# Kernel optimization log

Hardware: AMD Instinct MI355X
Metric: run time of the kernel (lower is better)

Reference implementation:

```python
import jax, jax.numpy as jnp
import numpy as np

NUM_HEADS = 8


def setup_inputs() -> dict:
    key = jax.random.key(0)
    k1, k2, k3 = jax.random.split(key, 3)
    B, N, C = 4, 8448, 512
    x = jax.random.normal(k1, (B, N, C), dtype=jnp.float32)
    w_qkv = jax.random.normal(k2, (3 * C, C), dtype=jnp.float32) * (C ** -0.5)
    w_proj = jax.random.normal(k3, (C, C), dtype=jnp.float32) * (C ** -0.5)
    b_proj = jnp.zeros((C,), dtype=jnp.float32)
    return {"x": x, "w_qkv": w_qkv, "w_proj": w_proj, "b_proj": b_proj, "N_points": 8192}


def reference(x, w_qkv, w_proj, b_proj, N_points):
    B, N, C = x.shape
    H = NUM_HEADS
    hd = C // H
    scale = hd ** -0.5
    N_latent = N - N_points

    qkv = (x @ w_qkv.T).reshape(B, N, 3, H, hd).transpose(2, 0, 3, 1, 4)  # [3,B,H,N,hd]
    q, k, v = qkv[0], qkv[1], qkv[2]
    q_l, k_l, v_l = q[:, :, :N_latent], k[:, :, :N_latent], v[:, :, :N_latent]
    q_p, k_p, v_p = q[:, :, N_latent:], k[:, :, N_latent:], v[:, :, N_latent:]

    # joint cross+self attention for the points
    attn_cross = jnp.einsum('bhpd,bhld->bhpl', q_p, k_l) * scale        # [B,H,P,L]
    attn_self = jnp.sum(q_p * k_p, axis=-1, keepdims=True) * scale      # [B,H,P,1]
    attn_joint = jax.nn.softmax(jnp.concatenate([attn_cross, attn_self], axis=-1), axis=-1)

    sum_cross = jnp.einsum('bhpl,bhld->bhpd', attn_joint[..., :N_latent], v_l)
    sum_self = attn_joint[..., N_latent:] * v_p
    out_points = (sum_cross + sum_self).transpose(0, 2, 1, 3).reshape(B, N_points, C)

    # standard self-attention over latent tokens
    attn_latent = jax.nn.softmax(jnp.einsum('bhqd,bhkd->bhqk', q_l, k_l) * scale, axis=-1)
    out_latent = jnp.einsum('bhqk,bhkd->bhqd', attn_latent, v_l).transpose(0, 2, 1, 3).reshape(B, N_latent, C)

    output = jnp.concatenate([out_latent, out_points], axis=1) @ w_proj.T + b_proj
    attn_mean = attn_joint[..., :-1].mean(axis=1)  # [B,P,L]
    return output, attn_mean
```

## Files before the change

kernel.cpp:

```cpp
#include <hip/hip_runtime.h>

#define BQ 4
#define NH 8
#define NTOK 8448
#define NLAT 256
#define NPTS 8192
#define CDIM 512
#define HD 64
#define SCALE 0.125f

typedef __attribute__((ext_vector_type(8))) short short8b;
typedef __attribute__((ext_vector_type(4))) float f32x4;

static __device__ __forceinline__ float4 ld4(const float* p) { return *(const float4*)p; }

static __device__ __forceinline__ short f2b(float f) {
  union { float f; unsigned u; } c; c.f = f;
  unsigned u = c.u;
  u += ((u >> 16) & 1u) + 0x7fffu;
  return (short)(u >> 16);
}

static __device__ __forceinline__ float b2f(unsigned short u) {
  union { unsigned u; float f; } c; c.u = ((unsigned)u) << 16; return c.f;
}

static __device__ __forceinline__ int cvtpk(float lo, float hi) {
  int r; asm("v_cvt_pk_bf16_f32 %0, %1, %2" : "=v"(r) : "v"(lo), "v"(hi)); return r;
}

static __device__ __forceinline__ void gload_lds16(const unsigned short* g, unsigned short* l) {
  __builtin_amdgcn_global_load_lds((const __attribute__((address_space(1))) void*)g,
                                   (__attribute__((address_space(3))) void*)l, 16, 0, 0);
}

__global__ __launch_bounds__(256) void to_bf16_3(const float* __restrict__ a, unsigned short* __restrict__ ao_, int na8,
                                                 const float* __restrict__ b, unsigned short* __restrict__ bo, int nb8,
                                                 const float* __restrict__ c, unsigned short* __restrict__ co, int nc8) {
  int i = blockIdx.x * 256 + threadIdx.x;
  const float* src; unsigned short* dst; int idx;
  if (i < na8) { src = a; dst = ao_; idx = i; }
  else if (i < na8 + nb8) { src = b; dst = bo; idx = i - na8; }
  else if (i < na8 + nb8 + nc8) { src = c; dst = co; idx = i - na8 - nb8; }
  else return;
  float4 x0 = ld4(src + (size_t)idx * 8);
  float4 x1 = ld4(src + (size_t)idx * 8 + 4);
  short8b r;
  r[0] = f2b(x0.x); r[1] = f2b(x0.y); r[2] = f2b(x0.z); r[3] = f2b(x0.w);
  r[4] = f2b(x1.x); r[5] = f2b(x1.y); r[6] = f2b(x1.z); r[7] = f2b(x1.w);
  *(short8b*)&dst[(size_t)idx * 8] = r;
}

#define STAGE128(PA, PB, kt, s)                                                              \
  do {                                                                                       \
    const int _c = (kt) * 64 + scell;                                                        \
    unsigned short* _d = &lds[(s) * 16384 + t * 8];                                          \
    gload_lds16((PA) + (size_t)(m0 + sr) * CDIM + _c,       _d);                             \
    gload_lds16((PA) + (size_t)(m0 + 32 + sr) * CDIM + _c,  _d + 2048);                      \
    gload_lds16((PA) + (size_t)(m0 + 64 + sr) * CDIM + _c,  _d + 4096);                      \
    gload_lds16((PA) + (size_t)(m0 + 96 + sr) * CDIM + _c,  _d + 6144);                      \
    gload_lds16((PB) + (size_t)(j0 + sr) * CDIM + _c,       _d + 8192);                      \
    gload_lds16((PB) + (size_t)(j0 + 32 + sr) * CDIM + _c,  _d + 10240);                     \
    gload_lds16((PB) + (size_t)(j0 + 64 + sr) * CDIM + _c,  _d + 12288);                     \
    gload_lds16((PB) + (size_t)(j0 + 96 + sr) * CDIM + _c,  _d + 14336);                     \
  } while (0)

#define GEMM128_BODY(PA, PB)                                                                 \
  __shared__ unsigned short lds[32768];                                                      \
  const int fl = blockIdx.y * gridDim.x + blockIdx.x;                                        \
  const int nchunk = (gridDim.x * gridDim.y) >> 3;                                           \
  const int wid = (fl & 7) * nchunk + (fl >> 3);                                             \
  const int m0 = (wid / gridDim.x) * 128;                                                    \
  const int j0 = (wid % gridDim.x) * 128;                                                    \
  const int t = threadIdx.x;                                                                 \
  const int lane = t & 63, wave = t >> 6;                                                    \
  const int wr = wave >> 1, wc = wave & 1;                                                   \
  const int lm = lane & 15, lq = lane >> 4;                                                  \
  const int sr = t >> 3;                                                                     \
  const int scell = (((t & 7) ^ (sr & 7)) << 3);                                             \
  f32x4 acc[4][4] = {};                                                                      \
  STAGE128(PA, PB, 0, 0);                                                                    \
  STAGE128(PA, PB, 1, 1);                                                                    \
  for (int kt = 0; kt < 8; ++kt) {                                                           \
    const int s = kt & 1;                                                                    \
    if (kt == 7) asm volatile("s_waitcnt vmcnt(0)" ::: "memory");                            \
    else         asm volatile("s_waitcnt vmcnt(8)" ::: "memory");                            \
    __builtin_amdgcn_s_barrier();                                                            \
    const unsigned short* sb = &lds[s * 16384];                                              \
    short8b af[4][2], bf[4][2];                                                              \
    _Pragma("unroll")                                                                        \
    for (int mt = 0; mt < 4; ++mt) {                                                         \
      const int RA = wr * 64 + mt * 16 + lm;                                                 \
      const int RB = wc * 64 + mt * 16 + lm;                                                 \
      af[mt][0] = *(const short8b*)&sb[RA * 64 + ((lq ^ (RA & 7)) << 3)];                    \
      af[mt][1] = *(const short8b*)&sb[RA * 64 + (((4 | lq) ^ (RA & 7)) << 3)];              \
      bf[mt][0] = *(const short8b*)&sb[8192 + RB * 64 + ((lq ^ (RB & 7)) << 3)];             \
      bf[mt][1] = *(const short8b*)&sb[8192 + RB * 64 + (((4 | lq) ^ (RB & 7)) << 3)];       \
    }                                                                                        \
    __builtin_amdgcn_s_setprio(1);                                                           \
    _Pragma("unroll")                                                                        \
    for (int ks = 0; ks < 2; ++ks)                                                           \
      _Pragma("unroll")                                                                      \
      for (int mt = 0; mt < 4; ++mt)                                                         \
        _Pragma("unroll")                                                                    \
        for (int nt = 0; nt < 4; ++nt)                                                       \
          acc[mt][nt] = __builtin_amdgcn_mfma_f32_16x16x32_bf16(af[mt][ks], bf[nt][ks],      \
                                                                acc[mt][nt], 0, 0, 0);       \
    __builtin_amdgcn_s_setprio(0);                                                           \
    asm volatile("s_waitcnt lgkmcnt(0)" ::: "memory");                                       \
    __builtin_amdgcn_s_barrier();                                                            \
    __builtin_amdgcn_sched_barrier(0);                                                       \
    if (kt < 6) STAGE128(PA, PB, kt + 2, s);                                                 \
  }

__global__ __launch_bounds__(256, 2) void qkv_mfma(const unsigned short* __restrict__ xb,
                                                   const unsigned short* __restrict__ wb,
                                                   unsigned short* __restrict__ qo,
                                                   unsigned short* __restrict__ ko,
                                                   unsigned short* __restrict__ vo) {
  GEMM128_BODY(xb, wb)
  const int s_ = j0 >> 9;
  unsigned short* dst = (s_ == 0) ? qo : ((s_ == 1) ? ko : vo);
  const int b = m0 / NTOK;
  const int n0 = m0 % NTOK;
  const int h = ((j0 >> 6) + wc) & 7;
#pragma unroll
  for (int mt = 0; mt < 4; ++mt) {
#pragma unroll
    for (int r = 0; r < 4; ++r) {
      const int n = n0 + wr * 64 + mt * 16 + lq * 4 + r;
      const size_t ob = (((size_t)b * NH + h) * NTOK + n) * HD;
#pragma unroll
      for (int nt = 0; nt < 4; ++nt)
        dst[ob + nt * 16 + lm] = (unsigned short)f2b(acc[mt][nt][r]);
    }
  }
}

__global__ __launch_bounds__(256, 2) void proj_mfma(const unsigned short* __restrict__ ab,
                                                    const unsigned short* __restrict__ wpb,
                                                    const float* __restrict__ bias,
                                                    float* __restrict__ out) {
  GEMM128_BODY(ab, wpb)
#pragma unroll
  for (int mt = 0; mt < 4; ++mt) {
#pragma unroll
    for (int r = 0; r < 4; ++r) {
      const int m = m0 + wr * 64 + mt * 16 + lq * 4 + r;
#pragma unroll
      for (int nt = 0; nt < 4; ++nt) {
        const int j = j0 + wc * 64 + nt * 16 + lm;
        out[(size_t)m * CDIM + j] = acc[mt][nt][r] + bias[j];
      }
    }
  }
}

__global__ __launch_bounds__(512, 2) void attn_pm(const unsigned short* __restrict__ qb,
                                                  const unsigned short* __restrict__ kb,
                                                  const unsigned short* __restrict__ vb,
                                                  unsigned short* __restrict__ aob,
                                                  float* __restrict__ out1) {
  __shared__ unsigned short kl[2][16384];
  __shared__ unsigned short vt[2][16384];
  const int t = threadIdx.x;
  const int lane = t & 63, wave = t >> 6;
  const int lm = lane & 15, lq = lane >> 4;
  if (blockIdx.x < 64) {
    const int idx = blockIdx.x;
    const int bh = idx >> 1, half = idx & 1;
    const size_t bhb = (size_t)bh * NTOK * HD;
    {
      const int vr = t >> 1, dh = t & 1;
      const unsigned short* vg = vb + bhb + (size_t)vr * HD + dh * 32;
      short8b rv[4];
#pragma unroll
      for (int i = 0; i < 4; ++i) rv[i] = *(const short8b*)(vg + i * 8);
      const int gsw = vr >> 3, wi = vr & 7;
#pragma unroll
      for (int i = 0; i < 4; ++i) {
        const int d0 = dh * 4 + i;
#pragma unroll
        for (int j = 0; j < 8; ++j)
          vt[0][(d0 * 8 + j) * 256 + ((gsw ^ j) << 3) + wi] = (unsigned short)rv[i][j];
      }
    }
    __syncthreads();
    const int b = bh >> 3, h = bh & 7;
    const int q0 = half * 128 + wave * 16;
    const size_t qrow = bhb + (size_t)(q0 + lm) * HD;
    const short8b bq0 = *(const short8b*)(qb + qrow + lq * 8);
    const short8b bq1 = *(const short8b*)(qb + qrow + 32 + lq * 8);
    f32x4 s[16] = {};
    __builtin_amdgcn_s_setprio(1);
#pragma unroll
    for (int mt = 0; mt < 16; ++mt) {
      const int krow = ((mt >> 1) << 5) + ((lm >> 2) << 3) + ((mt & 1) << 2) + (lm & 3);
      const unsigned short* kr = kb + bhb + (size_t)krow * HD + lq * 8;
      s[mt] = __builtin_amdgcn_mfma_f32_16x16x32_bf16(*(const short8b*)kr, bq0, s[mt], 0, 0, 0);
      s[mt] = __builtin_amdgcn_mfma_f32_16x16x32_bf16(*(const short8b*)(kr + 32), bq1, s[mt], 0, 0, 0);
    }
    __builtin_amdgcn_s_setprio(0);
    float mx = -1e30f;
#pragma unroll
    for (int mt = 0; mt < 16; ++mt)
#pragma unroll
      for (int r = 0; r < 4; ++r) mx = fmaxf(mx, s[mt][r]);
    mx = fmaxf(mx, __shfl_xor(mx, 16));
    mx = fmaxf(mx, __shfl_xor(mx, 32));
    const float m = mx * SCALE;
    float sum = 0.f;
#pragma unroll
    for (int mt = 0; mt < 16; ++mt)
#pragma unroll
      for (int r = 0; r < 4; ++r) {
        float e = __expf(fmaf(s[mt][r], SCALE, -m));
        s[mt][r] = e;
        sum += e;
      }
    sum += __shfl_xor(sum, 16);
    sum += __shfl_xor(sum, 32);
    const float inv = 1.f / sum;
#pragma unroll
    for (int mt = 0; mt < 16; ++mt)
#pragma unroll
      for (int r = 0; r < 4; ++r) s[mt][r] *= inv;
    f32x4 o[4] = {};
    __builtin_amdgcn_s_setprio(1);
#pragma unroll
    for (int ks = 0; ks < 8; ++ks) {
      union { int i[4]; short8b v; } af;
      af.i[0] = cvtpk(s[2 * ks][0], s[2 * ks][1]);
      af.i[1] = cvtpk(s[2 * ks][2], s[2 * ks][3]);
      af.i[2] = cvtpk(s[2 * ks + 1][0], s[2 * ks + 1][1]);
      af.i[3] = cvtpk(s[2 * ks + 1][2], s[2 * ks + 1][3]);
#pragma unroll
      for (int ntd = 0; ntd < 4; ++ntd) {
        const int row = ntd * 16 + lm;
        const short8b bv = *(const short8b*)&vt[0][row * 256 + ((((ks << 2) | lq) ^ (lm & 7)) << 3)];
        o[ntd] = __builtin_amdgcn_mfma_f32_16x16x32_bf16(af.v, bv, o[ntd], 0, 0, 0);
      }
    }
    __builtin_amdgcn_s_setprio(0);
#pragma unroll
    for (int ntd = 0; ntd < 4; ++ntd)
#pragma unroll
      for (int r = 0; r < 4; ++r) {
        const int n = q0 + lq * 4 + r;
        aob[((size_t)b * NTOK + n) * CDIM + h * HD + ntd * 16 + lm] =
            (unsigned short)f2b(o[ntd][r]);
      }
    return;
  }
  const int bidx = blockIdx.x - 64;
  const int b = bidx >> 6, pq = bidx & 63;
  const int pp0 = pq * 128 + wave * 16;
  const size_t bb = (size_t)(b * NH) * NTOK * HD;
  const int vr = t >> 1, dh = t & 1;
  const int gsw = vr >> 3, wi = vr & 7;
  short8b vregs[4];
#define ISSUE_K(hh, sl_)                                                          \
  do {                                                                            \
    const unsigned short* kg = kb + bb + (size_t)(hh) * NTOK * HD;                \
    _Pragma("unroll")                                                             \
    for (int c = 0; c < 4; ++c) {                                                 \
      const int rr = c * 64 + (t >> 3);                                           \
      const int mt_ = rr >> 4, w_ = rr & 15;                                      \
      const int g = 32 * (mt_ >> 1) + 8 * (w_ >> 2) + 4 * (mt_ & 1) + (w_ & 3);   \
      gload_lds16(kg + g * HD + (((t & 7) ^ (rr & 7)) << 3),                      \
                  &kl[sl_][(c * 512 + t) * 8]);                                   \
    }                                                                             \
  } while (0)
#define READ_V(hh)                                                                \
  do {                                                                            \
    const unsigned short* vg = vb + bb + (size_t)(hh) * NTOK * HD +               \
                               (size_t)vr * HD + dh * 32;                         \
    _Pragma("unroll")                                                             \
    for (int i = 0; i < 4; ++i) vregs[i] = *(const short8b*)(vg + i * 8);         \
  } while (0)
#define WRITE_V(sl_)                                                              \
  do {                                                                            \
    _Pragma("unroll")                                                             \
    for (int i = 0; i < 4; ++i) {                                                 \
      const int d0 = dh * 4 + i;                                                  \
      _Pragma("unroll")                                                           \
      for (int j = 0; j < 8; ++j)                                                 \
        vt[sl_][(d0 * 8 + j) * 256 + ((gsw ^ j) << 3) + wi] =                     \
            (unsigned short)vregs[i][j];                                          \
    }                                                                             \
  } while (0)
  f32x4 prob[16] = {};
  ISSUE_K(0, 0); READ_V(0);
  asm volatile("s_waitcnt vmcnt(0)" ::: "memory");
  WRITE_V(0);
  ISSUE_K(1, 1); READ_V(1);
  __syncthreads();
  for (int h = 0; h < NH; ++h) {
    const int sl = h & 1;
    const size_t hb = bb + (size_t)h * NTOK * HD;
    const size_t qrow = hb + (size_t)(NLAT + pp0 + lm) * HD;
    const short8b bq0 = *(const short8b*)(qb + qrow + lq * 8);
    const short8b bq1 = *(const short8b*)(qb + qrow + 32 + lq * 8);
    f32x4 s[16] = {};
    __builtin_amdgcn_s_setprio(1);
#pragma unroll
    for (int mt = 0; mt < 16; ++mt) {
      const int rr = mt * 16 + lm;
      const short8b ak0 = *(const short8b*)&kl[sl][rr * 64 + ((lq ^ (rr & 7)) << 3)];
      const short8b ak1 = *(const short8b*)&kl[sl][rr * 64 + (((4 | lq) ^ (rr & 7)) << 3)];
      s[mt] = __builtin_amdgcn_mfma_f32_16x16x32_bf16(ak0, bq0, s[mt], 0, 0, 0);
      s[mt] = __builtin_amdgcn_mfma_f32_16x16x32_bf16(ak1, bq1, s[mt], 0, 0, 0);
    }
    __builtin_amdgcn_s_setprio(0);
    float sself = 0.f;
    {
      const unsigned short* qp = qb + qrow + lq * 16;
      const unsigned short* kp = kb + qrow + lq * 16;
      short8b q0 = *(const short8b*)qp, q1 = *(const short8b*)(qp + 8);
      short8b k0 = *(const short8b*)kp, k1 = *(const short8b*)(kp + 8);
#pragma unroll
      for (int j = 0; j < 8; ++j)
        sself += b2f((unsigned short)q0[j]) * b2f((unsigned short)k0[j]) +
                 b2f((unsigned short)q1[j]) * b2f((unsigned short)k1[j]);
    }
    sself += __shfl_xor(sself, 16);
    sself += __shfl_xor(sself, 32);
    sself *= SCALE;
    float mx = -1e30f;
#pragma unroll
    for (int mt = 0; mt < 16; ++mt)
#pragma unroll
      for (int r = 0; r < 4; ++r) mx = fmaxf(mx, s[mt][r]);
    mx = fmaxf(mx, __shfl_xor(mx, 16));
    mx = fmaxf(mx, __shfl_xor(mx, 32));
    const float m = fmaxf(mx * SCALE, sself);
    float sum = 0.f;
#pragma unroll
    for (int mt = 0; mt < 16; ++mt)
#pragma unroll
      for (int r = 0; r < 4; ++r) {
        float e = __expf(fmaf(s[mt][r], SCALE, -m));
        s[mt][r] = e;
        sum += e;
      }
    sum += __shfl_xor(sum, 16);
    sum += __shfl_xor(sum, 32);
    const float pself = __expf(sself - m);
    const float inv = 1.f / (sum + pself);
#pragma unroll
    for (int mt = 0; mt < 16; ++mt)
#pragma unroll
      for (int r = 0; r < 4; ++r) {
        const float pn = s[mt][r] * inv;
        s[mt][r] = pn;
        prob[mt][r] += pn;
      }
    f32x4 o[4] = {};
    __builtin_amdgcn_s_setprio(1);
#pragma unroll
    for (int ks = 0; ks < 8; ++ks) {
      union { int i[4]; short8b v; } af;
      af.i[0] = cvtpk(s[2 * ks][0], s[2 * ks][1]);
      af.i[1] = cvtpk(s[2 * ks][2], s[2 * ks][3]);
      af.i[2] = cvtpk(s[2 * ks + 1][0], s[2 * ks + 1][1]);
      af.i[3] = cvtpk(s[2 * ks + 1][2], s[2 * ks + 1][3]);
#pragma unroll
      for (int ntd = 0; ntd < 4; ++ntd) {
        const int row = ntd * 16 + lm;
        const short8b bv = *(const short8b*)&vt[sl][row * 256 + ((((ks << 2) | lq) ^ (lm & 7)) << 3)];
        o[ntd] = __builtin_amdgcn_mfma_f32_16x16x32_bf16(af.v, bv, o[ntd], 0, 0, 0);
      }
    }
    __builtin_amdgcn_s_setprio(0);
    const float pisl = pself * inv;
    float psl[4];
#pragma unroll
    for (int r = 0; r < 4; ++r) psl[r] = __shfl(pisl, lq * 4 + r);
#pragma unroll
    for (int ntd = 0; ntd < 4; ++ntd)
#pragma unroll
      for (int r = 0; r < 4; ++r) {
        const int n = NLAT + pp0 + lq * 4 + r;
        const float v_ = b2f(vb[hb + (size_t)n * HD + ntd * 16 + lm]);
        aob[((size_t)b * NTOK + n) * CDIM + h * HD + ntd * 16 + lm] =
            (unsigned short)f2b(o[ntd][r] + psl[r] * v_);
      }
    __syncthreads();
    if (h < 7) {
      asm volatile("s_waitcnt vmcnt(0)" ::: "memory");
      WRITE_V(sl ^ 1);
      if (h < 6) { ISSUE_K(h + 2, sl); READ_V(h + 2); }
      __syncthreads();
    }
  }
  const size_t orow = ((size_t)b * NPTS + pp0 + lm) * NLAT;
#pragma unroll
  for (int mt = 0; mt < 16; ++mt) {
    const int col = 32 * (mt >> 1) + 8 * lq + 4 * (mt & 1);
    *(float4*)&out1[orow + col] = make_float4(prob[mt][0] * 0.125f, prob[mt][1] * 0.125f,
                                              prob[mt][2] * 0.125f, prob[mt][3] * 0.125f);
  }
#undef ISSUE_K
#undef READ_V
#undef WRITE_V
}

extern "C" void kernel_launch(void* const* d_in, const int* in_sizes, int n_in,
                              void* d_out, int out_size, void* d_ws, size_t ws_size,
                              hipStream_t stream) {
  const float* x      = (const float*)d_in[0];
  const float* w_qkv  = (const float*)d_in[1];
  const float* w_proj = (const float*)d_in[2];
  const float* b_proj = (const float*)d_in[3];
  const size_t QSZ = (size_t)BQ * NH * NTOK * HD;
  unsigned short* qb  = (unsigned short*)d_ws;
  unsigned short* kb  = qb + QSZ;
  unsigned short* vb  = kb + QSZ;
  unsigned short* aob = vb + QSZ;
  unsigned short* xb  = aob + QSZ;
  unsigned short* wb  = xb + QSZ;
  unsigned short* wpb = wb + 786432;
  float* out0 = (float*)d_out;
  float* out1 = out0 + (size_t)BQ * NTOK * CDIM;

  to_bf16_3<<<8960, 256, 0, stream>>>(x, xb, 2162688, w_qkv, wb, 98304, w_proj, wpb, 32768);
  qkv_mfma<<<dim3(12, 264), 256, 0, stream>>>(xb, wb, qb, kb, vb);
  attn_pm<<<320, 512, 0, stream>>>(qb, kb, vb, aob, out1);
  proj_mfma<<<dim3(4, 264), 256, 0, stream>>>(aob, wpb, b_proj, out0);
}
```

Baseline: 184.6 us.

## Single-buffer K/V LDS to double occupancy, reorder blocks, use exp2 softmax

Drops the double-buffered K and V shared-memory tiles in the fused attention kernel to a single buffer and raises launch bounds from 2 to 4 blocks per CU, so more waves can hide latency. The next head's K is now loaded only after a barrier at the end of each head, which removes the prefetch overlap across heads. Point blocks are remapped so neighbouring block IDs spread across batch and query chunks, and the latent blocks move to the end of the grid. Softmax switches from __expf to exp2f with log2(e) folded into the scale.

```diff
diff --git a/kernel.cpp b/kernel.cpp
--- a/kernel.cpp
+++ b/kernel.cpp
@@ -8,6 +8,8 @@
 #define CDIM 512
 #define HD 64
 #define SCALE 0.125f
+#define L2E 1.4426950408889634f
+#define SC2 0.1803368801111204f
 
 typedef __attribute__((ext_vector_type(8))) short short8b;
 typedef __attribute__((ext_vector_type(4))) float f32x4;
@@ -156,18 +158,18 @@
   }
 }
 
-__global__ __launch_bounds__(512, 2) void attn_pm(const unsigned short* __restrict__ qb,
+__global__ __launch_bounds__(512, 4) void attn_pm(const unsigned short* __restrict__ qb,
                                                   const unsigned short* __restrict__ kb,
                                                   const unsigned short* __restrict__ vb,
                                                   unsigned short* __restrict__ aob,
                                                   float* __restrict__ out1) {
-  __shared__ unsigned short kl[2][16384];
-  __shared__ unsigned short vt[2][16384];
+  __shared__ unsigned short kl[16384];
+  __shared__ unsigned short vt[16384];
   const int t = threadIdx.x;
   const int lane = t & 63, wave = t >> 6;
   const int lm = lane & 15, lq = lane >> 4;
-  if (blockIdx.x < 64) {
-    const int idx = blockIdx.x;
+  if (blockIdx.x >= 256) {
+    const int idx = blockIdx.x - 256;
     const int bh = idx >> 1, half = idx & 1;
     const size_t bhb = (size_t)bh * NTOK * HD;
     {
@@ -182,7 +184,7 @@
         const int d0 = dh * 4 + i;
 #pragma unroll
         for (int j = 0; j < 8; ++j)
-          vt[0][(d0 * 8 + j) * 256 + ((gsw ^ j) << 3) + wi] = (unsigned short)rv[i][j];
+          vt[(d0 * 8 + j) * 256 + ((gsw ^ j) << 3) + wi] = (unsigned short)rv[i][j];
       }
     }
     __syncthreads();
@@ -208,13 +210,13 @@
       for (int r = 0; r < 4; ++r) mx = fmaxf(mx, s[mt][r]);
     mx = fmaxf(mx, __shfl_xor(mx, 16));
     mx = fmaxf(mx, __shfl_xor(mx, 32));
-    const float m = mx * SCALE;
+    const float m2 = mx * SCALE * L2E;
     float sum = 0.f;
 #pragma unroll
     for (int mt = 0; mt < 16; ++mt)
 #pragma unroll
       for (int r = 0; r < 4; ++r) {
-        float e = __expf(fmaf(s[mt][r], SCALE, -m));
+        float e = exp2f(fmaf(s[mt][r], SC2, -m2));
         s[mt][r] = e;
         sum += e;
       }
@@ -237,7 +239,7 @@
 #pragma unroll
       for (int ntd = 0; ntd < 4; ++ntd) {
         const int row = ntd * 16 + lm;
-        const short8b bv = *(const short8b*)&vt[0][row * 256 + ((((ks << 2) | lq) ^ (lm & 7)) << 3)];
+        const short8b bv = *(const short8b*)&vt[row * 256 + ((((ks << 2) | lq) ^ (lm & 7)) << 3)];
         o[ntd] = __builtin_amdgcn_mfma_f32_16x16x32_bf16(af.v, bv, o[ntd], 0, 0, 0);
       }
     }
@@ -252,14 +254,15 @@
       }
     return;
   }
-  const int bidx = blockIdx.x - 64;
-  const int b = bidx >> 6, pq = bidx & 63;
+  const int fl = blockIdx.x;
+  const int wid = (fl & 7) * 32 + (fl >> 3);
+  const int b = wid >> 6, pq = wid & 63;
   const int pp0 = pq * 128 + wave * 16;
   const size_t bb = (size_t)(b * NH) * NTOK * HD;
   const int vr = t >> 1, dh = t & 1;
   const int gsw = vr >> 3, wi = vr & 7;
   short8b vregs[4];
-#define ISSUE_K(hh, sl_)                                                          \
+#define ISSUE_K(hh)                                                               \
   do {                                                                            \
     const unsigned short* kg = kb + bb + (size_t)(hh) * NTOK * HD;                \
     _Pragma("unroll")                                                             \
@@ -267,8 +270,7 @@
       const int rr = c * 64 + (t >> 3);                                           \
       const int mt_ = rr >> 4, w_ = rr & 15;                                      \
       const int g = 32 * (mt_ >> 1) + 8 * (w_ >> 2) + 4 * (mt_ & 1) + (w_ & 3);   \
-      gload_lds16(kg + g * HD + (((t & 7) ^ (rr & 7)) << 3),                      \
-                  &kl[sl_][(c * 512 + t) * 8]);                                   \
+      gload_lds16(kg + g * HD + (((t & 7) ^ (rr & 7)) << 3), &kl[(c * 512 + t) * 8]); \
     }                                                                             \
   } while (0)
 #define READ_V(hh)                                                                \
@@ -278,25 +280,23 @@
     _Pragma("unroll")                                                             \
     for (int i = 0; i < 4; ++i) vregs[i] = *(const short8b*)(vg + i * 8);         \
   } while (0)
-#define WRITE_V(sl_)                                                              \
+#define WRITE_V()                                                                 \
   do {                                                                            \
     _Pragma("unroll")                                                             \
     for (int i = 0; i < 4; ++i) {                                                 \
       const int d0 = dh * 4 + i;                                                  \
       _Pragma("unroll")                                                           \
       for (int j = 0; j < 8; ++j)                                                 \
-        vt[sl_][(d0 * 8 + j) * 256 + ((gsw ^ j) << 3) + wi] =                     \
-            (unsigned short)vregs[i][j];                                          \
+        vt[(d0 * 8 + j) * 256 + ((gsw ^ j) << 3) + wi] = (unsigned short)vregs[i][j]; \
     }                                                                             \
   } while (0)
   f32x4 prob[16] = {};
-  ISSUE_K(0, 0); READ_V(0);
+  ISSUE_K(0); READ_V(0);
   asm volatile("s_waitcnt vmcnt(0)" ::: "memory");
-  WRITE_V(0);
-  ISSUE_K(1, 1); READ_V(1);
+  WRITE_V();
   __syncthreads();
   for (int h = 0; h < NH; ++h) {
-    const int sl = h & 1;
+    if (h < 7) READ_V(h + 1);
     const size_t hb = bb + (size_t)h * NTOK * HD;
     const size_t qrow = hb + (size_t)(NLAT + pp0 + lm) * HD;
     const short8b bq0 = *(const short8b*)(qb + qrow + lq * 8);
@@ -306,8 +306,8 @@
 #pragma unroll
     for (int mt = 0; mt < 16; ++mt) {
       const int rr = mt * 16 + lm;
-      const short8b ak0 = *(const short8b*)&kl[sl][rr * 64 + ((lq ^ (rr & 7)) << 3)];
-      const short8b ak1 = *(const short8b*)&kl[sl][rr * 64 + (((4 | lq) ^ (rr & 7)) << 3)];
+      const short8b ak0 = *(const short8b*)&kl[rr * 64 + ((lq ^ (rr & 7)) << 3)];
+      const short8b ak1 = *(const short8b*)&kl[rr * 64 + (((4 | lq) ^ (rr & 7)) << 3)];
       s[mt] = __builtin_amdgcn_mfma_f32_16x16x32_bf16(ak0, bq0, s[mt], 0, 0, 0);
       s[mt] = __builtin_amdgcn_mfma_f32_16x16x32_bf16(ak1, bq1, s[mt], 0, 0, 0);
     }
@@ -334,18 +334,19 @@
     mx = fmaxf(mx, __shfl_xor(mx, 16));
     mx = fmaxf(mx, __shfl_xor(mx, 32));
     const float m = fmaxf(mx * SCALE, sself);
+    const float m2 = m * L2E;
     float sum = 0.f;
 #pragma unroll
     for (int mt = 0; mt < 16; ++mt)
 #pragma unroll
       for (int r = 0; r < 4; ++r) {
-        float e = __expf(fmaf(s[mt][r], SCALE, -m));
+        float e = exp2f(fmaf(s[mt][r], SC2, -m2));
         s[mt][r] = e;
         sum += e;
       }
     sum += __shfl_xor(sum, 16);
     sum += __shfl_xor(sum, 32);
-    const float pself = __expf(sself - m);
+    const float pself = exp2f(fmaf(sself, L2E, -m2));
     const float inv = 1.f / (sum + pself);
 #pragma unroll
     for (int mt = 0; mt < 16; ++mt)
@@ -367,7 +368,7 @@
 #pragma unroll
       for (int ntd = 0; ntd < 4; ++ntd) {
         const int row = ntd * 16 + lm;
-        const short8b bv = *(const short8b*)&vt[sl][row * 256 + ((((ks << 2) | lq) ^ (lm & 7)) << 3)];
+        const short8b bv = *(const short8b*)&vt[row * 256 + ((((ks << 2) | lq) ^ (lm & 7)) << 3)];
         o[ntd] = __builtin_amdgcn_mfma_f32_16x16x32_bf16(af.v, bv, o[ntd], 0, 0, 0);
       }
     }
@@ -385,11 +386,11 @@
         aob[((size_t)b * NTOK + n) * CDIM + h * HD + ntd * 16 + lm] =
             (unsigned short)f2b(o[ntd][r] + psl[r] * v_);
       }
-    __syncthreads();
     if (h < 7) {
+      __syncthreads();
+      ISSUE_K(h + 1);
       asm volatile("s_waitcnt vmcnt(0)" ::: "memory");
-      WRITE_V(sl ^ 1);
-      if (h < 6) { ISSUE_K(h + 2, sl); READ_V(h + 2); }
+      WRITE_V();
       __syncthreads();
     }
   }
```

Measured after the change: 321.3 us. 74.1% more time.

## Pre-transpose latent V into global buffer and read it directly in attention

Applied to the files above, without the earlier changes.

Adds a small vtrans kernel that writes the swizzled transposed latent V for each (batch, head) to a workspace buffer. The attention kernel then reads V fragments straight from global/L2 instead of staging them through LDS, which halves LDS use and drops the V read/write pipeline and some barriers. Softmax exponentials are also rewritten as exp2 with a prescaled log2(e) factor. The cost is an extra kernel launch, and the P·V MFMA operands now come from uncached-in-LDS global loads, which may add latency.

```diff
diff --git a/kernel.cpp b/kernel.cpp
--- a/kernel.cpp
+++ b/kernel.cpp
@@ -8,6 +8,8 @@
 #define CDIM 512
 #define HD 64
 #define SCALE 0.125f
+#define L2E 1.4426950408889634f
+#define SC2 0.1803368801111204f
 
 typedef __attribute__((ext_vector_type(8))) short short8b;
 typedef __attribute__((ext_vector_type(4))) float f32x4;
@@ -49,6 +51,23 @@
   r[0] = f2b(x0.x); r[1] = f2b(x0.y); r[2] = f2b(x0.z); r[3] = f2b(x0.w);
   r[4] = f2b(x1.x); r[5] = f2b(x1.y); r[6] = f2b(x1.z); r[7] = f2b(x1.w);
   *(short8b*)&dst[(size_t)idx * 8] = r;
+}
+
+__global__ __launch_bounds__(256) void vtrans(const unsigned short* __restrict__ vb,
+                                              unsigned short* __restrict__ vtg) {
+  const int bh = blockIdx.x;
+  const int n = threadIdx.x;
+  const unsigned short* vr = vb + (size_t)bh * NTOK * HD + (size_t)n * HD;
+  short8b rv[8];
+#pragma unroll
+  for (int i = 0; i < 8; ++i) rv[i] = *(const short8b*)(vr + i * 8);
+  unsigned short* dst = vtg + (size_t)bh * 16384;
+  const int gsw = n >> 3, wi = n & 7;
+#pragma unroll
+  for (int d0 = 0; d0 < 8; ++d0)
+#pragma unroll
+    for (int j = 0; j < 8; ++j)
+      dst[(d0 * 8 + j) * 256 + ((gsw ^ j) << 3) + wi] = (unsigned short)rv[d0][j];
 }
 
 #define STAGE128(PA, PB, kt, s)                                                              \
@@ -159,10 +178,10 @@
 __global__ __launch_bounds__(512, 2) void attn_pm(const unsigned short* __restrict__ qb,
                                                   const unsigned short* __restrict__ kb,
                                                   const unsigned short* __restrict__ vb,
+                                                  const unsigned short* __restrict__ vtg,
                                                   unsigned short* __restrict__ aob,
                                                   float* __restrict__ out1) {
   __shared__ unsigned short kl[2][16384];
-  __shared__ unsigned short vt[2][16384];
   const int t = threadIdx.x;
   const int lane = t & 63, wave = t >> 6;
   const int lm = lane & 15, lq = lane >> 4;
@@ -170,22 +189,7 @@
     const int idx = blockIdx.x;
     const int bh = idx >> 1, half = idx & 1;
     const size_t bhb = (size_t)bh * NTOK * HD;
-    {
-      const int vr = t >> 1, dh = t & 1;
-      const unsigned short* vg = vb + bhb + (size_t)vr * HD + dh * 32;
-      short8b rv[4];
-#pragma unroll
-      for (int i = 0; i < 4; ++i) rv[i] = *(const short8b*)(vg + i * 8);
-      const int gsw = vr >> 3, wi = vr & 7;
-#pragma unroll
-      for (int i = 0; i < 4; ++i) {
-        const int d0 = dh * 4 + i;
-#pragma unroll
-        for (int j = 0; j < 8; ++j)
-          vt[0][(d0 * 8 + j) * 256 + ((gsw ^ j) << 3) + wi] = (unsigned short)rv[i][j];
-      }
-    }
-    __syncthreads();
+    const unsigned short* vtp = vtg + (size_t)bh * 16384;
     const int b = bh >> 3, h = bh & 7;
     const int q0 = half * 128 + wave * 16;
     const size_t qrow = bhb + (size_t)(q0 + lm) * HD;
@@ -208,13 +212,13 @@
       for (int r = 0; r < 4; ++r) mx = fmaxf(mx, s[mt][r]);
     mx = fmaxf(mx, __shfl_xor(mx, 16));
     mx = fmaxf(mx, __shfl_xor(mx, 32));
-    const float m = mx * SCALE;
+    const float m2 = mx * SCALE * L2E;
     float sum = 0.f;
 #pragma unroll
     for (int mt = 0; mt < 16; ++mt)
 #pragma unroll
       for (int r = 0; r < 4; ++r) {
-        float e = __expf(fmaf(s[mt][r], SCALE, -m));
+        float e = exp2f(fmaf(s[mt][r], SC2, -m2));
         s[mt][r] = e;
         sum += e;
       }
@@ -237,7 +241,7 @@
 #pragma unroll
       for (int ntd = 0; ntd < 4; ++ntd) {
         const int row = ntd * 16 + lm;
-        const short8b bv = *(const short8b*)&vt[0][row * 256 + ((((ks << 2) | lq) ^ (lm & 7)) << 3)];
+        const short8b bv = *(const short8b*)&vtp[row * 256 + ((((ks << 2) | lq) ^ (lm & 7)) << 3)];
         o[ntd] = __builtin_amdgcn_mfma_f32_16x16x32_bf16(af.v, bv, o[ntd], 0, 0, 0);
       }
     }
@@ -252,13 +256,10 @@
       }
     return;
   }
-  const int bidx = blockIdx.x - 64;
-  const int b = bidx >> 6, pq = bidx & 63;
+  const int wid = blockIdx.x - 64;
+  const int b = wid >> 6, pq = wid & 63;
   const int pp0 = pq * 128 + wave * 16;
   const size_t bb = (size_t)(b * NH) * NTOK * HD;
-  const int vr = t >> 1, dh = t & 1;
-  const int gsw = vr >> 3, wi = vr & 7;
-  short8b vregs[4];
 #define ISSUE_K(hh, sl_)                                                          \
   do {                                                                            \
     const unsigned short* kg = kb + bb + (size_t)(hh) * NTOK * HD;                \
@@ -271,34 +272,16 @@
                   &kl[sl_][(c * 512 + t) * 8]);                                   \
     }                                                                             \
   } while (0)
-#define READ_V(hh)                                                                \
-  do {                                                                            \
-    const unsigned short* vg = vb + bb + (size_t)(hh) * NTOK * HD +               \
-                               (size_t)vr * HD + dh * 32;                         \
-    _Pragma("unroll")                                                             \
-    for (int i = 0; i < 4; ++i) vregs[i] = *(const short8b*)(vg + i * 8);         \
-  } while (0)
-#define WRITE_V(sl_)                                                              \
-  do {                                                                            \
-    _Pragma("unroll")                                                             \
-    for (int i = 0; i < 4; ++i) {                                                 \
-      const int d0 = dh * 4 + i;                                                  \
-      _Pragma("unroll")                                                           \
-      for (int j = 0; j < 8; ++j)                                                 \
-        vt[sl_][(d0 * 8 + j) * 256 + ((gsw ^ j) << 3) + wi] =                     \
-            (unsigned short)vregs[i][j];                                          \
-    }                                                                             \
-  } while (0)
   f32x4 prob[16] = {};
-  ISSUE_K(0, 0); READ_V(0);
+  ISSUE_K(0, 0);
+  ISSUE_K(1, 1);
   asm volatile("s_waitcnt vmcnt(0)" ::: "memory");
-  WRITE_V(0);
-  ISSUE_K(1, 1); READ_V(1);
-  __syncthreads();
+  __builtin_amdgcn_s_barrier();
   for (int h = 0; h < NH; ++h) {
     const int sl = h & 1;
     const size_t hb = bb + (size_t)h * NTOK * HD;
     const size_t qrow = hb + (size_t)(NLAT + pp0 + lm) * HD;
+    const unsigned short* vtp = vtg + (size_t)(b * NH + h) * 16384;
     const short8b bq0 = *(const short8b*)(qb + qrow + lq * 8);
     const short8b bq1 = *(const short8b*)(qb + qrow + 32 + lq * 8);
     f32x4 s[16] = {};
@@ -334,18 +317,19 @@
     mx = fmaxf(mx, __shfl_xor(mx, 16));
     mx = fmaxf(mx, __shfl_xor(mx, 32));
     const float m = fmaxf(mx * SCALE, sself);
+    const float m2 = m * L2E;
     float sum = 0.f;
 #pragma unroll
     for (int mt = 0; mt < 16; ++mt)
 #pragma unroll
       for (int r = 0; r < 4; ++r) {
-        float e = __expf(fmaf(s[mt][r], SCALE, -m));
+        float e = exp2f(fmaf(s[mt][r], SC2, -m2));
         s[mt][r] = e;
         sum += e;
       }
     sum += __shfl_xor(sum, 16);
     sum += __shfl_xor(sum, 32);
-    const float pself = __expf(sself - m);
+    const float pself = exp2f(fmaf(sself, L2E, -m2));
     const float inv = 1.f / (sum + pself);
 #pragma unroll
     for (int mt = 0; mt < 16; ++mt)
@@ -367,7 +351,7 @@
 #pragma unroll
       for (int ntd = 0; ntd < 4; ++ntd) {
         const int row = ntd * 16 + lm;
-        const short8b bv = *(const short8b*)&vt[sl][row * 256 + ((((ks << 2) | lq) ^ (lm & 7)) << 3)];
+        const short8b bv = *(const short8b*)&vtp[row * 256 + ((((ks << 2) | lq) ^ (lm & 7)) << 3)];
         o[ntd] = __builtin_amdgcn_mfma_f32_16x16x32_bf16(af.v, bv, o[ntd], 0, 0, 0);
       }
     }
@@ -385,12 +369,11 @@
         aob[((size_t)b * NTOK + n) * CDIM + h * HD + ntd * 16 + lm] =
             (unsigned short)f2b(o[ntd][r] + psl[r] * v_);
       }
-    __syncthreads();
+    __builtin_amdgcn_s_barrier();
     if (h < 7) {
       asm volatile("s_waitcnt vmcnt(0)" ::: "memory");
-      WRITE_V(sl ^ 1);
-      if (h < 6) { ISSUE_K(h + 2, sl); READ_V(h + 2); }
-      __syncthreads();
+      if (h < 6) ISSUE_K(h + 2, sl);
+      __builtin_amdgcn_s_barrier();
     }
   }
   const size_t orow = ((size_t)b * NPTS + pp0 + lm) * NLAT;
@@ -401,8 +384,6 @@
                                               prob[mt][2] * 0.125f, prob[mt][3] * 0.125f);
   }
 #undef ISSUE_K
-#undef READ_V
-#undef WRITE_V
 }
 
 extern "C" void kernel_launch(void* const* d_in, const int* in_sizes, int n_in,
@@ -420,11 +401,13 @@
   unsigned short* xb  = aob + QSZ;
   unsigned short* wb  = xb + QSZ;
   unsigned short* wpb = wb + 786432;
+  unsigned short* vtg = wpb + 262144;
   float* out0 = (float*)d_out;
   float* out1 = out0 + (size_t)BQ * NTOK * CDIM;
 
   to_bf16_3<<<8960, 256, 0, stream>>>(x, xb, 2162688, w_qkv, wb, 98304, w_proj, wpb, 32768);
   qkv_mfma<<<dim3(12, 264), 256, 0, stream>>>(xb, wb, qb, kb, vb);
-  attn_pm<<<320, 512, 0, stream>>>(qb, kb, vb, aob, out1);
+  vtrans<<<32, 256, 0, stream>>>(vb, vtg);
+  attn_pm<<<320, 512, 0, stream>>>(qb, kb, vb, vtg, aob, out1);
   proj_mfma<<<dim3(4, 264), 256, 0, stream>>>(aob, wpb, b_proj, out0);
 }
```

Measured after the change: 202.0 us. +9.4%, slower.
